# Kernel tuning notes

Measured on AMD Instinct MI355X. Metric: run time of the kernel, lower is better.

## Reference

```python
import jax, jax.numpy as jnp
import numpy as np

EPS = 1e-5  # torch BatchNorm1d default eps


def _bn(x, p):
    # eval-mode batchnorm; p = stacked [gamma, beta, running_mean, running_var], shape [4, C]
    g, b, m, v = p
    return (x - m[:, None]) * jax.lax.rsqrt(v[:, None] + EPS) * g[:, None] + b[:, None]


def _conv(w, x):
    # 1x1 Conv1d == channel matmul: w [O,C], x [B,C,N] -> [B,O,N]
    return jnp.einsum('oc,bcn->bon', w, x)


def _sa(x, qk_w, v_w, v_b, t_w, t_b, bnp):
    # offset self-attention; q_conv.weight is tied to k_conv.weight in the original
    q = jnp.einsum('oc,bcn->bno', qk_w, x)          # [B,N,C/4]
    k = _conv(qk_w, x)                              # [B,C/4,N]
    v = _conv(v_w, x) + v_b[None, :, None]          # [B,C,N]
    attn = jax.nn.softmax(jnp.einsum('bno,bom->bnm', q, k), axis=-1)  # [B,N,N]
    attn = attn / (1e-9 + attn.sum(axis=1, keepdims=True))            # L1 re-norm over dim 1
    x_r = jnp.einsum('bcn,bnm->bcm', v, attn)       # [B,C,N]
    x_r = jax.nn.relu(_bn(_conv(t_w, x - x_r) + t_b[None, :, None], bnp))
    return x + x_r


def setup_inputs():
    key = jax.random.key(0)
    ks = iter(jax.random.split(key, 64))
    def n(shape, s=0.1):
        return jax.random.normal(next(ks), shape, jnp.float32) * s
    def bn_p(c):
        g = jax.random.uniform(next(ks), (c,), jnp.float32, 0.5, 1.5)
        b = n((c,))
        m = n((c,))
        v = jax.random.uniform(next(ks), (c,), jnp.float32, 0.5, 1.5)
        return jnp.stack([g, b, m, v])
    B, C, N = 16, 16, 2048
    return {
        'x': jax.random.normal(next(ks), (B, C, N), jnp.float32),
        'conv1_w': n((128, 16)), 'bn1': bn_p(128),
        'conv2_w': n((16, 128)), 'bn2': bn_p(16),
        'sa_qk_w': n((4, 4, 16)), 'sa_v_w': n((4, 16, 16)), 'sa_v_b': n((4, 16)),
        'sa_trans_w': n((4, 16, 16)), 'sa_trans_b': n((4, 16)),
        'sa_bn': jnp.stack([bn_p(16) for _ in range(4)]),
        'fuse_w': n((128, 64)), 'fuse_bn': bn_p(128),
        'convs1_w': n((512, 264)), 'convs1_b': n((512,)), 'bns1': bn_p(512),
        'convs2_w': n((256, 512)), 'convs2_b': n((256,)), 'bns2': bn_p(256),
        'convs3_w': n((16, 256)), 'convs3_b': n((16,)),
    }


def reference(x, conv1_w, bn1, conv2_w, bn2, sa_qk_w, sa_v_w, sa_v_b,
              sa_trans_w, sa_trans_b, sa_bn, fuse_w, fuse_bn,
              convs1_w, convs1_b, bns1, convs2_w, convs2_b, bns2,
              convs3_w, convs3_b):
    B, _, N = x.shape
    h = jax.nn.relu(_bn(_conv(conv1_w, x), bn1))   # [B,128,N]
    h = jax.nn.relu(_bn(_conv(conv2_w, h), bn2))   # [B,16,N]
    feats = []
    for i in range(4):
        h = _sa(h, sa_qk_w[i], sa_v_w[i], sa_v_b[i], sa_trans_w[i], sa_trans_b[i], sa_bn[i])
        feats.append(h)
    xqq = jnp.concatenate(feats, axis=1)           # [B,64,N]
    xqqw = jax.nn.leaky_relu(_bn(_conv(fuse_w, xqq), fuse_bn), 0.2)  # [B,128,N]
    # faithful to original (including the [1]-indexing quirk):
    x_max = jnp.argmax(xqqw, axis=2)               # [B,128] argmax indices (torch.max(...)[1])
    x_avg = jnp.mean(xqqw, axis=2)[1]              # [128] batch element 1's channel means
    x_max_f = jnp.broadcast_to(x_max.astype(jnp.float32)[:, :, None], (B, 128, N))
    x_avg_f = jnp.broadcast_to(x_avg.reshape(B, -1)[:, :, None], (B, 128 // B, N))
    g = jnp.concatenate([xqqw, x_max_f, x_avg_f], axis=1)  # [B,264,N]
    g = jax.nn.relu(_bn(_conv(convs1_w, g) + convs1_b[None, :, None], bns1))
    # dropout is identity in eval mode
    g = jax.nn.relu(_bn(_conv(convs2_w, g) + convs2_b[None, :, None], bns2))
    return _conv(convs3_w, g) + convs3_b[None, :, None]  # [B,16,N]
```

## Files before the change

kernel.cpp:

```cpp
#include <hip/hip_runtime.h>
#include <stdint.h>

typedef __bf16 bf16_t;
typedef __bf16 bf16x8 __attribute__((ext_vector_type(8)));
typedef __bf16 bf16x4 __attribute__((ext_vector_type(4)));
typedef float f32x4 __attribute__((ext_vector_type(4)));
typedef float f32x2 __attribute__((ext_vector_type(2)));

#define LOG2E 1.4426950408889634f

__device__ __forceinline__ float relu_(float v) { return v > 0.f ? v : 0.f; }

__global__ __launch_bounds__(256) void k_prep(
    const float* __restrict__ convs1_w, const float* __restrict__ convs2_w,
    const float* __restrict__ bn1, const float* __restrict__ bn2,
    const float* __restrict__ sa_bn, const float* __restrict__ sa_trans_b,
    const float* __restrict__ fuse_bn, const float* __restrict__ convs1_b,
    const float* __restrict__ bns1, const float* __restrict__ convs2_b,
    const float* __restrict__ bns2,
    bf16_t* __restrict__ wbuf1, bf16_t* __restrict__ wbuf2, float* __restrict__ params)
{
  int idx = blockIdx.x * 256 + threadIdx.x;
  for (int it = 0; it < 3; ++it) {
    int i = idx + it * 65536;
    if (i < 65536) {
      int o = i >> 7, c = i & 127;
      wbuf1[i] = (bf16_t)convs1_w[o * 264 + c];
    } else if (i < 65536 + 131072) {
      int j = i - 65536;
      wbuf2[j] = (bf16_t)convs2_w[j];
    }
  }
  if (blockIdx.x == 0) {
    for (int t = threadIdx.x; t < 1104; t += 256) {
      float g, be, m, v, extra = 0.f; int so, ho;
      if (t < 128)      { g=bn1[t]; be=bn1[128+t]; m=bn1[256+t]; v=bn1[384+t]; so=t; ho=128+t; }
      else if (t < 144) { int u=t-128; g=bn2[u]; be=bn2[16+u]; m=bn2[32+u]; v=bn2[48+u]; so=256+u; ho=272+u; }
      else if (t < 208) { int u=t-144; int L=u>>4, o=u&15; const float* p=sa_bn+L*64;
                          g=p[o]; be=p[16+o]; m=p[32+o]; v=p[48+o];
                          extra=sa_trans_b[L*16+o]; so=288+u; ho=352+u; }
      else if (t < 336) { int u=t-208; g=fuse_bn[u]; be=fuse_bn[128+u]; m=fuse_bn[256+u]; v=fuse_bn[384+u]; so=416+u; ho=544+u; }
      else if (t < 848) { int u=t-336; g=bns1[u]; be=bns1[512+u]; m=bns1[1024+u]; v=bns1[1536+u]; extra=convs1_b[u]; so=672+u; ho=1184+u; }
      else              { int u=t-848; g=bns2[u]; be=bns2[256+u]; m=bns2[512+u]; v=bns2[768+u]; extra=convs2_b[u]; so=1696+u; ho=1952+u; }
      float sc = g * rsqrtf(v + 1e-5f);
      params[so] = sc;
      params[ho] = (extra - m) * sc + be;
    }
  }
}

__global__ __launch_bounds__(256) void k_convs(const float* __restrict__ x,
    const float* __restrict__ w1, const float* __restrict__ w2,
    const float* __restrict__ params, const float* __restrict__ qk_w,
    const float* __restrict__ v_w, const float* __restrict__ v_b,
    float* __restrict__ h0, float* __restrict__ kbuf, float* __restrict__ vbufT)
{
  __shared__ __align__(16) float xs[16 * 128];
  __shared__ float ws1[128 * 17];
  __shared__ float ws2[16 * 129];
  __shared__ __align__(16) float h1s[128 * 64];
  __shared__ float hcv[128 * 17];
  __shared__ float qk[64], vw[256], vb[16], sc1[128], sh1[128], sc2[16], sh2[16];
  int t = threadIdx.x;
  int bid = blockIdx.x;
  int b = bid >> 4, n0 = (bid & 15) * 128;
  for (int i = t; i < 2048; i += 256) { int c = i >> 7, col = i & 127; xs[c * 128 + col] = x[((size_t)b * 16 + c) * 2048 + n0 + col]; }
  for (int i = t; i < 2048; i += 256) { int o = i >> 4, c = i & 15;  ws1[o * 17 + c]  = w1[i]; }
  for (int i = t; i < 2048; i += 256) { int o = i >> 7, c = i & 127; ws2[o * 129 + c] = w2[i]; }
  if (t < 64) qk[t] = qk_w[t];
  vw[t] = v_w[t];
  if (t < 16) { vb[t] = v_b[t]; sc2[t] = params[256 + t]; sh2[t] = params[272 + t]; }
  if (t < 128) { sc1[t] = params[t]; sh1[t] = params[128 + t]; }
  __syncthreads();
  int colh = t & 63, hi4 = t >> 6;
  int cg = t & 15, og = t >> 4;
  for (int h = 0; h < 2; ++h) {
    int cb = h * 64;
    float xr[16];
#pragma unroll
    for (int c = 0; c < 16; ++c) xr[c] = xs[c * 128 + cb + colh];
#pragma unroll 4
    for (int i = 0; i < 32; ++i) {
      int o = (i << 2) | hi4;
      float s = 0.f;
#pragma unroll
      for (int c = 0; c < 16; ++c) s = fmaf(ws1[o * 17 + c], xr[c], s);
      h1s[o * 64 + colh] = relu_(fmaf(s, sc1[o], sh1[o]));
    }
    __syncthreads();
    float a0 = 0.f, a1 = 0.f, a2 = 0.f, a3 = 0.f;
    for (int c = 0; c < 128; ++c) {
      float4 f = *(const float4*)&h1s[c * 64 + cg * 4];
      float w = ws2[og * 129 + c];
      a0 = fmaf(w, f.x, a0); a1 = fmaf(w, f.y, a1);
      a2 = fmaf(w, f.z, a2); a3 = fmaf(w, f.w, a3);
    }
    float4 v4;
    v4.x = relu_(fmaf(a0, sc2[og], sh2[og]));
    v4.y = relu_(fmaf(a1, sc2[og], sh2[og]));
    v4.z = relu_(fmaf(a2, sc2[og], sh2[og]));
    v4.w = relu_(fmaf(a3, sc2[og], sh2[og]));
    *(float4*)&h0[((size_t)b * 16 + og) * 2048 + n0 + cb + cg * 4] = v4;
    hcv[(cb + cg * 4 + 0) * 17 + og] = v4.x;
    hcv[(cb + cg * 4 + 1) * 17 + og] = v4.y;
    hcv[(cb + cg * 4 + 2) * 17 + og] = v4.z;
    hcv[(cb + cg * 4 + 3) * 17 + og] = v4.w;
    __syncthreads();
  }
  int col = t & 127, ug = t >> 7;
  float hr[16];
#pragma unroll
  for (int c = 0; c < 16; ++c) hr[c] = hcv[col * 17 + c];
#pragma unroll
  for (int i = 0; i < 10; ++i) {
    int u = ug * 10 + i;
    const float* W = (u < 4) ? &qk[u * 16] : &vw[(u - 4) * 16];
    float s = (u < 4) ? 0.f : vb[u - 4];
#pragma unroll
    for (int c = 0; c < 16; ++c) s = fmaf(W[c], hr[c], s);
    if (u < 4) kbuf[((size_t)b * 2048 + n0 + col) * 4 + u] = s;
    else       vbufT[((size_t)b * 2048 + n0 + col) * 16 + (u - 4)] = s;
  }
}

__global__ __launch_bounds__(256) void k_rowstats(const float* __restrict__ kbuf, float* __restrict__ Lpart)
{
  __shared__ float4 kch[256];
  int bid = blockIdx.x;
  int b = bid >> 6, nt = (bid >> 3) & 7, ms = bid & 7;
  int t = threadIdx.x;
  const float4* kb = (const float4*)kbuf + b * 2048;
  kch[t] = kb[ms * 256 + t];
  __syncthreads();
  int n = nt * 256 + t;
  float4 q = kb[n];
  q.x *= LOG2E; q.y *= LOG2E; q.z *= LOG2E; q.w *= LOG2E;
  float L = 0.f;
#pragma unroll 4
  for (int m = 0; m < 256; ++m) {
    float4 k4 = kch[m];
    float s = fmaf(q.x, k4.x, fmaf(q.y, k4.y, fmaf(q.z, k4.z, q.w * k4.w)));
    L += exp2f(s);
  }
  Lpart[((size_t)ms * 16 + b) * 2048 + n] = L;
}

__global__ __launch_bounds__(256) void k_colaccum(const float* __restrict__ kbuf, const float* __restrict__ vbufT,
    const float* __restrict__ Lpart, float* __restrict__ parts)
{
  __shared__ __align__(16) float ku[256 * 8];
  __shared__ __align__(16) float vch[256 * 16];
  int bid = blockIdx.x;
  int b = bid >> 5, mt = (bid >> 3) & 3, ns = bid & 7;
  int t = threadIdx.x;
  {
    int n = ns * 256 + t;
    float4 k4 = ((const float4*)kbuf)[b * 2048 + n];
    float Ls = 0.f;
#pragma unroll
    for (int s = 0; s < 8; ++s) Ls += Lpart[((size_t)s * 16 + b) * 2048 + n];
    *(float4*)&ku[t * 8] = k4;
    ku[t * 8 + 4] = -__log2f(Ls);
    const float4* vp = (const float4*)&vbufT[((size_t)b * 2048 + n) * 16];
    *(float4*)&vch[t * 16 + 0]  = vp[0];
    *(float4*)&vch[t * 16 + 4]  = vp[1];
    *(float4*)&vch[t * 16 + 8]  = vp[2];
    *(float4*)&vch[t * 16 + 12] = vp[3];
  }
  __syncthreads();
  int m0 = mt * 512 + t;
  float4 qa = ((const float4*)kbuf)[b * 2048 + m0];
  float4 qb = ((const float4*)kbuf)[b * 2048 + m0 + 256];
  qa.x *= LOG2E; qa.y *= LOG2E; qa.z *= LOG2E; qa.w *= LOG2E;
  qb.x *= LOG2E; qb.y *= LOG2E; qb.z *= LOG2E; qb.w *= LOG2E;
  f32x2 acc0[8], acc1[8];
#pragma unroll
  for (int j = 0; j < 8; ++j) { acc0[j] = (f32x2){0.f, 0.f}; acc1[j] = (f32x2){0.f, 0.f}; }
  float den0 = 0.f, den1 = 0.f;
#pragma unroll 2
  for (int nn = 0; nn < 256; ++nn) {
    f32x4 k4 = *(const f32x4*)&ku[nn * 8];
    float lg = ku[nn * 8 + 4];
    float s0 = fmaf(qa.x, k4[0], fmaf(qa.y, k4[1], fmaf(qa.z, k4[2], fmaf(qa.w, k4[3], lg))));
    float s1 = fmaf(qb.x, k4[0], fmaf(qb.y, k4[1], fmaf(qb.z, k4[2], fmaf(qb.w, k4[3], lg))));
    float e0 = exp2f(s0), e1 = exp2f(s1);
    den0 += e0; den1 += e1;
    f32x2 ev0 = {e0, e0}, ev1 = {e1, e1};
    const f32x2* vp = (const f32x2*)&vch[nn * 16];
#pragma unroll
    for (int j = 0; j < 8; ++j) { f32x2 v2 = vp[j]; acc0[j] += ev0 * v2; acc1[j] += ev1 * v2; }
  }
  float* p = parts + ((size_t)(ns * 16 + b) * 17) * 2048 + m0;
#pragma unroll
  for (int c = 0; c < 16; ++c) p[(size_t)c * 2048] = acc0[c >> 1][c & 1];
  p[(size_t)16 * 2048] = den0;
  p += 256;
#pragma unroll
  for (int c = 0; c < 16; ++c) p[(size_t)c * 2048] = acc1[c >> 1][c & 1];
  p[(size_t)16 * 2048] = den1;
}

__global__ __launch_bounds__(256) void k_epilogue(const float* __restrict__ parts,
    const float* __restrict__ hin, int hbs, const float* __restrict__ t_w,
    const float* __restrict__ params, int layer, float* __restrict__ hout,
    const float* __restrict__ qk_w, const float* __restrict__ v_w, const float* __restrict__ v_b,
    float* __restrict__ kbuf, float* __restrict__ vbufT)
{
  __shared__ float pd[17 * 64];
  __shared__ float hs[16 * 64];
  __shared__ float dl[16 * 64];
  __shared__ float hv[64 * 17];
  __shared__ float tw[256], qk[64], vw[256], vb[16], sc[16], sh[16];
  int t = threadIdx.x;
  int bid = blockIdx.x;
  int b = bid >> 5, n0 = (bid & 31) * 64;
  tw[t] = t_w[t];
  if (qk_w) { if (t < 64) qk[t] = qk_w[t]; vw[t] = v_w[t]; if (t < 16) vb[t] = v_b[t]; }
  if (t < 16) { sc[t] = params[288 + layer * 16 + t]; sh[t] = params[352 + layer * 16 + t]; }
  for (int i = t; i < 1088; i += 256) {
    int r = i >> 6, c = i & 63;
    float s = 0.f;
#pragma unroll
    for (int sp = 0; sp < 8; ++sp)
      s += parts[((size_t)(sp * 16 + b) * 17 + r) * 2048 + n0 + c];
    pd[i] = s;
  }
  for (int i = t; i < 1024; i += 256) {
    int c = i >> 6, col = i & 63;
    hs[i] = hin[(size_t)b * hbs + (size_t)c * 2048 + n0 + col];
  }
  __syncthreads();
  int col = t & 63, g4 = t >> 6;
  float inv = 1.f / (1e-9f + pd[16 * 64 + col]);
#pragma unroll
  for (int j = 0; j < 4; ++j) {
    int c = g4 * 4 + j;
    dl[c * 64 + col] = hs[c * 64 + col] - pd[c * 64 + col] * inv;
  }
  __syncthreads();
#pragma unroll
  for (int j = 0; j < 4; ++j) {
    int o = g4 * 4 + j;
    float y = 0.f;
#pragma unroll
    for (int c = 0; c < 16; ++c) y = fmaf(tw[o * 16 + c], dl[c * 64 + col], y);
    y = relu_(fmaf(y, sc[o], sh[o]));
    float hh = hs[o * 64 + col] + y;
    hout[(size_t)b * 64 * 2048 + (size_t)o * 2048 + n0 + col] = hh;
    hv[col * 17 + o] = hh;
  }
  if (qk_w) {
    __syncthreads();
    float hr[16];
#pragma unroll
    for (int c = 0; c < 16; ++c) hr[c] = hv[col * 17 + c];
#pragma unroll
    for (int i = 0; i < 5; ++i) {
      int u = g4 * 5 + i;
      const float* W = (u < 4) ? &qk[u * 16] : &vw[(u - 4) * 16];
      float s = (u < 4) ? 0.f : vb[u - 4];
#pragma unroll
      for (int c = 0; c < 16; ++c) s = fmaf(W[c], hr[c], s);
      if (u < 4) kbuf[((size_t)b * 2048 + n0 + col) * 4 + u] = s;
      else       vbufT[((size_t)b * 2048 + n0 + col) * 16 + (u - 4)] = s;
    }
  }
}

__global__ __launch_bounds__(256) void k_fuse(const float* __restrict__ feats, const float* __restrict__ fw,
    const float* __restrict__ params, float* __restrict__ xqqw, bf16_t* __restrict__ gbuf)
{
  __shared__ float ws[128 * 65];
  __shared__ __align__(16) float fst[64 * 64];
  __shared__ float sc[128], sh[128];
  int t = threadIdx.x, bid = blockIdx.x;
  int b = bid >> 5, n0 = (bid & 31) * 64;
  for (int i = t; i < 8192; i += 256) { int o = i >> 6, c = i & 63; ws[o * 65 + c] = fw[i]; }
  for (int i = t; i < 4096; i += 256) { int c = i >> 6, col = i & 63; fst[i] = feats[((size_t)b * 64 + c) * 2048 + n0 + col]; }
  if (t < 128) { sc[t] = params[416 + t]; sh[t] = params[544 + t]; }
  __syncthreads();
  int cg = t & 7, og = t >> 3;
  f32x2 acc[4][4];
#pragma unroll
  for (int oo = 0; oo < 4; ++oo)
#pragma unroll
    for (int j = 0; j < 4; ++j) acc[oo][j] = (f32x2){0.f, 0.f};
  for (int c = 0; c < 64; ++c) {
    const f32x2* fp = (const f32x2*)&fst[c * 64 + cg * 8];
    f32x2 f0 = fp[0], f1 = fp[1], f2v = fp[2], f3 = fp[3];
#pragma unroll
    for (int oo = 0; oo < 4; ++oo) {
      float w = ws[(og * 4 + oo) * 65 + c];
      f32x2 wv = {w, w};
      acc[oo][0] += wv * f0; acc[oo][1] += wv * f1;
      acc[oo][2] += wv * f2v; acc[oo][3] += wv * f3;
    }
  }
  float y[4][8];
#pragma unroll
  for (int oo = 0; oo < 4; ++oo) {
    int o = og * 4 + oo;
    float s0 = sc[o], s1 = sh[o];
#pragma unroll
    for (int j = 0; j < 8; ++j) {
      float v = fmaf(acc[oo][j >> 1][j & 1], s0, s1);
      y[oo][j] = v > 0.f ? v : 0.2f * v;
    }
    float4 v0 = {y[oo][0], y[oo][1], y[oo][2], y[oo][3]};
    float4 v1 = {y[oo][4], y[oo][5], y[oo][6], y[oo][7]};
    *(float4*)&xqqw[((size_t)b * 128 + o) * 2048 + n0 + cg * 8] = v0;
    *(float4*)&xqqw[((size_t)b * 128 + o) * 2048 + n0 + cg * 8 + 4] = v1;
  }
#pragma unroll
  for (int j = 0; j < 8; ++j) {
    int col = n0 + cg * 8 + j;
    bf16x4 pk;
    pk[0] = (bf16_t)y[0][j]; pk[1] = (bf16_t)y[1][j];
    pk[2] = (bf16_t)y[2][j]; pk[3] = (bf16_t)y[3][j];
    *(bf16x4*)&gbuf[((size_t)b * 2048 + col) * 128 + og * 4] = pk;
  }
}

__global__ __launch_bounds__(256) void k_argmax(const float* __restrict__ xqqw,
    float* __restrict__ xmaxf, float* __restrict__ xavg)
{
  __shared__ float sv[256]; __shared__ int si[256]; __shared__ float ss[256];
  int bo = blockIdx.x;
  int b = bo >> 7, o = bo & 127;
  const float* row = xqqw + (size_t)bo * 2048;
  int tid = threadIdx.x;
  float best = -3.4e38f; int bi = 0; float sum = 0.f;
#pragma unroll
  for (int j = 0; j < 8; ++j) {
    int n = j * 256 + tid;
    float v = row[n];
    sum += v;
    if (v > best) { best = v; bi = n; }
  }
  sv[tid] = best; si[tid] = bi; ss[tid] = sum;
  __syncthreads();
  for (int s = 128; s > 0; s >>= 1) {
    if (tid < s) {
      float v2 = sv[tid + s]; int i2 = si[tid + s];
      if (v2 > sv[tid] || (v2 == sv[tid] && i2 < si[tid])) { sv[tid] = v2; si[tid] = i2; }
      ss[tid] += ss[tid + s];
    }
    __syncthreads();
  }
  if (tid == 0) {
    xmaxf[bo] = (float)si[0];
    if (b == 1) xavg[o] = ss[0] * (1.0f / 2048.0f);
  }
}

__global__ __launch_bounds__(256) void k_bias2(const float* __restrict__ w1,
    const float* __restrict__ xmaxf, const float* __restrict__ xavg,
    const float* __restrict__ params, float* __restrict__ bias2)
{
  int id = blockIdx.x * 256 + threadIdx.x;
  int o = id >> 4, b = id & 15;
  const float* wr = w1 + (size_t)o * 264;
  float s = 0.f;
  for (int u = 0; u < 128; ++u) s = fmaf(wr[128 + u], xmaxf[b * 128 + u], s);
#pragma unroll
  for (int u = 0; u < 8; ++u)  s = fmaf(wr[256 + u], xavg[b * 8 + u], s);
  bias2[b * 512 + o] = s * params[672 + o];
}

__global__ __launch_bounds__(256) void k_gemm(const bf16_t* __restrict__ A, const bf16_t* __restrict__ Bm,
    const float* __restrict__ scp, const float* __restrict__ shp, const float* __restrict__ bias2,
    bf16_t* __restrict__ Cout, int M, int K, int mtiles)
{
  __shared__ bf16_t At[128 * 32];
  __shared__ bf16_t Bt[128 * 32];
  int tid = threadIdx.x;
  int mt = blockIdx.x % mtiles, ct = blockIdx.x / mtiles;
  int srow = tid >> 2, scol = (tid & 3) << 3;
  const bf16_t* ga = A  + (size_t)(mt * 128 + srow) * K + scol;
  const bf16_t* gb = Bm + (size_t)(ct * 128 + srow) * K + scol;
  int lane = tid & 63, wave = tid >> 6;
  int wr = (wave >> 1) * 64, wc = (wave & 1) * 64;
  int frow = lane & 15, fk = (lane >> 4) * 8;
  const f32x4 z4 = {0.f, 0.f, 0.f, 0.f};
  f32x4 acc[4][4];
#pragma unroll
  for (int i = 0; i < 4; ++i)
#pragma unroll
    for (int j = 0; j < 4; ++j) acc[i][j] = z4;
  uint4 ra0 = *(const uint4*)ga, ra1 = *(const uint4*)(ga + (size_t)64 * K);
  uint4 rb0 = *(const uint4*)gb, rb1 = *(const uint4*)(gb + (size_t)64 * K);
  int ksteps = K >> 5;
  for (int ks = 0; ks < ksteps; ++ks) {
    __syncthreads();
    *(uint4*)&At[tid * 8] = ra0;  *(uint4*)&At[2048 + tid * 8] = ra1;
    *(uint4*)&Bt[tid * 8] = rb0;  *(uint4*)&Bt[2048 + tid * 8] = rb1;
    __syncthreads();
    if (ks + 1 < ksteps) {
      ra0 = *(const uint4*)(ga + (ks + 1) * 32);
      ra1 = *(const uint4*)(ga + (size_t)64 * K + (ks + 1) * 32);
      rb0 = *(const uint4*)(gb + (ks + 1) * 32);
      rb1 = *(const uint4*)(gb + (size_t)64 * K + (ks + 1) * 32);
    }
    bf16x8 af[4], bfr[4];
#pragma unroll
    for (int i = 0; i < 4; ++i) af[i]  = *(const bf16x8*)&At[(wr + i * 16 + frow) * 32 + fk];
#pragma unroll
    for (int j = 0; j < 4; ++j) bfr[j] = *(const bf16x8*)&Bt[(wc + j * 16 + frow) * 32 + fk];
#pragma unroll
    for (int i = 0; i < 4; ++i)
#pragma unroll
      for (int j = 0; j < 4; ++j)
        acc[i][j] = __builtin_amdgcn_mfma_f32_16x16x32_bf16(af[i], bfr[j], acc[i][j], 0, 0, 0);
  }
  int crow = (lane >> 4) * 4, ccol = lane & 15;
#pragma unroll
  for (int i = 0; i < 4; ++i) {
    int o0 = mt * 128 + wr + i * 16 + crow;
    float s0 = scp[o0], s1 = scp[o0+1], s2 = scp[o0+2], s3 = scp[o0+3];
    float t0 = shp[o0], t1 = shp[o0+1], t2 = shp[o0+2], t3 = shp[o0+3];
#pragma unroll
    for (int j = 0; j < 4; ++j) {
      int bn = ct * 128 + wc + j * 16 + ccol;
      float b0 = 0.f, b1 = 0.f, b2 = 0.f, b3 = 0.f;
      if (bias2) {
        const float* bp = bias2 + (size_t)(bn >> 11) * M + o0;
        b0 = bp[0]; b1 = bp[1]; b2 = bp[2]; b3 = bp[3];
      }
      bf16x4 pk;
      pk[0] = (bf16_t)relu_(fmaf(acc[i][j][0], s0, t0 + b0));
      pk[1] = (bf16_t)relu_(fmaf(acc[i][j][1], s1, t1 + b1));
      pk[2] = (bf16_t)relu_(fmaf(acc[i][j][2], s2, t2 + b2));
      pk[3] = (bf16_t)relu_(fmaf(acc[i][j][3], s3, t3 + b3));
      *(bf16x4*)(Cout + (size_t)bn * M + o0) = pk;
    }
  }
}

__global__ __launch_bounds__(128) void k_gemm3(const bf16_t* __restrict__ g2, const float* __restrict__ w3,
    const float* __restrict__ b3, float* __restrict__ out)
{
  __shared__ float wsT[4096];
  __shared__ float bb[16];
  int tid = threadIdx.x;
  for (int i = tid; i < 4096; i += 128) { int o = i >> 8, k = i & 255; wsT[k * 16 + o] = w3[i]; }
  if (tid < 16) bb[tid] = b3[tid];
  __syncthreads();
  int col = blockIdx.x * 128 + tid;
  int b = col >> 11, n = col & 2047;
  const bf16_t* g = g2 + (size_t)col * 256;
  float acc[16];
#pragma unroll
  for (int o = 0; o < 16; ++o) acc[o] = 0.f;
  for (int k0 = 0; k0 < 256; k0 += 8) {
    bf16x8 gv8 = *(const bf16x8*)(g + k0);
#pragma unroll
    for (int kk = 0; kk < 8; ++kk) {
      float gv = (float)gv8[kk];
      const float* wr = &wsT[(k0 + kk) * 16];
#pragma unroll
      for (int o = 0; o < 16; ++o) acc[o] = fmaf(wr[o], gv, acc[o]);
    }
  }
  float* op = out + (size_t)b * 16 * 2048 + n;
#pragma unroll
  for (int o = 0; o < 16; ++o) op[(size_t)o * 2048] = acc[o] + bb[o];
}

extern "C" void kernel_launch(void* const* d_in, const int* in_sizes, int n_in,
                              void* d_out, int out_size, void* d_ws, size_t ws_size,
                              hipStream_t stream)
{
  const float* x         = (const float*)d_in[0];
  const float* conv1_w   = (const float*)d_in[1];
  const float* bn1       = (const float*)d_in[2];
  const float* conv2_w   = (const float*)d_in[3];
  const float* bn2       = (const float*)d_in[4];
  const float* sa_qk_w   = (const float*)d_in[5];
  const float* sa_v_w    = (const float*)d_in[6];
  const float* sa_v_b    = (const float*)d_in[7];
  const float* sa_trans_w= (const float*)d_in[8];
  const float* sa_trans_b= (const float*)d_in[9];
  const float* sa_bn     = (const float*)d_in[10];
  const float* fuse_w    = (const float*)d_in[11];
  const float* fuse_bn   = (const float*)d_in[12];
  const float* convs1_w  = (const float*)d_in[13];
  const float* convs1_b  = (const float*)d_in[14];
  const float* bns1      = (const float*)d_in[15];
  const float* convs2_w  = (const float*)d_in[16];
  const float* convs2_b  = (const float*)d_in[17];
  const float* bns2      = (const float*)d_in[18];
  const float* convs3_w  = (const float*)d_in[19];
  const float* convs3_b  = (const float*)d_in[20];

  char* ws = (char*)d_ws;
  float*  xqqw  = (float*)(ws + 0);
  float*  feats = (float*)(ws + 16777216);
  float*  h0    = (float*)(ws + 25165824);
  float*  kbuf  = (float*)(ws + 27262976);
  float*  vbufT = (float*)(ws + 27787264);
  float*  Lpart = (float*)(ws + 29884416);
  float*  parts = (float*)(ws + 30932992);
  bf16_t* gbuf  = (bf16_t*)(ws + 48758784);
  bf16_t* g2    = (bf16_t*)(ws + 57147392);
  bf16_t* g1    = (bf16_t*)(ws + 0);
  bf16_t* wbuf1 = (bf16_t*)(ws + 73924608);
  bf16_t* wbuf2 = (bf16_t*)(ws + 74055680);
  float*  params= (float*)(ws + 74317824);
  float*  xmaxf = (float*)(ws + 74334208);
  float*  xavg  = (float*)(ws + 74342400);
  float*  bias2 = (float*)(ws + 74346496);

  k_prep<<<256, 256, 0, stream>>>(convs1_w, convs2_w, bn1, bn2, sa_bn, sa_trans_b, fuse_bn,
                                  convs1_b, bns1, convs2_b, bns2, wbuf1, wbuf2, params);
  k_convs<<<256, 256, 0, stream>>>(x, conv1_w, conv2_w, params, sa_qk_w, sa_v_w, sa_v_b,
                                   h0, kbuf, vbufT);
  for (int i = 0; i < 4; ++i) {
    k_rowstats<<<1024, 256, 0, stream>>>(kbuf, Lpart);
    k_colaccum<<<512, 256, 0, stream>>>(kbuf, vbufT, Lpart, parts);
    const float* hin = (i == 0) ? h0 : (feats + (size_t)(i - 1) * 16 * 2048);
    int hbs = (i == 0) ? 16 * 2048 : 64 * 2048;
    bool last = (i == 3);
    k_epilogue<<<512, 256, 0, stream>>>(parts, hin, hbs, sa_trans_w + i * 256, params, i,
        feats + (size_t)i * 16 * 2048,
        last ? nullptr : sa_qk_w + (i + 1) * 64,
        last ? nullptr : sa_v_w + (i + 1) * 256,
        last ? nullptr : sa_v_b + (i + 1) * 16,
        kbuf, vbufT);
  }
  k_fuse<<<512, 256, 0, stream>>>(feats, fuse_w, params, xqqw, gbuf);
  k_argmax<<<2048, 256, 0, stream>>>(xqqw, xmaxf, xavg);
  k_bias2<<<32, 256, 0, stream>>>(convs1_w, xmaxf, xavg, params, bias2);
  k_gemm<<<1024, 256, 0, stream>>>(wbuf1, gbuf, params + 672, params + 1184, bias2, g1, 512, 128, 4);
  k_gemm<<<512, 256, 0, stream>>>(wbuf2, g1, params + 1696, params + 1952, nullptr, g2, 256, 512, 2);
  k_gemm3<<<256, 128, 0, stream>>>(g2, convs3_w, convs3_b, (float*)d_out);
}
```

Measured before the change: 551.9 us.

## Double grid sizes across conv, attention and final GEMM kernels for more parallelism

Halves the per-block work tile in k_convs, k_rowstats, k_colaccum and k_gemm3 and doubles their grid sizes, splitting the attention key dimension into 16 partial slices instead of 8. The epilogue sums 16 partials using vectorized float4 loads, k_colaccum spreads its shared-memory staging across both thread halves, and its V loads become explicit float4 reads. The workspace layout is rearranged to hold the larger partials buffer. The goal is to fill more compute units and raise occupancy, at the cost of more partial-sum traffic and reduction work.

After: 518.3 us. -6.1%, faster.

```diff
diff --git a/kernel.cpp b/kernel.cpp
--- a/kernel.cpp
+++ b/kernel.cpp
@@ -55,16 +55,16 @@
     const float* __restrict__ v_w, const float* __restrict__ v_b,
     float* __restrict__ h0, float* __restrict__ kbuf, float* __restrict__ vbufT)
 {
-  __shared__ __align__(16) float xs[16 * 128];
+  __shared__ float xs[16 * 64];
   __shared__ float ws1[128 * 17];
   __shared__ float ws2[16 * 129];
   __shared__ __align__(16) float h1s[128 * 64];
-  __shared__ float hcv[128 * 17];
+  __shared__ float hcv[64 * 17];
   __shared__ float qk[64], vw[256], vb[16], sc1[128], sh1[128], sc2[16], sh2[16];
   int t = threadIdx.x;
   int bid = blockIdx.x;
-  int b = bid >> 4, n0 = (bid & 15) * 128;
-  for (int i = t; i < 2048; i += 256) { int c = i >> 7, col = i & 127; xs[c * 128 + col] = x[((size_t)b * 16 + c) * 2048 + n0 + col]; }
+  int b = bid >> 5, n0 = (bid & 31) * 64;
+  for (int i = t; i < 1024; i += 256) { int c = i >> 6, col = i & 63; xs[i] = x[((size_t)b * 16 + c) * 2048 + n0 + col]; }
   for (int i = t; i < 2048; i += 256) { int o = i >> 4, c = i & 15;  ws1[o * 17 + c]  = w1[i]; }
   for (int i = t; i < 2048; i += 256) { int o = i >> 7, c = i & 127; ws2[o * 129 + c] = w2[i]; }
   if (t < 64) qk[t] = qk_w[t];
@@ -72,48 +72,39 @@
   if (t < 16) { vb[t] = v_b[t]; sc2[t] = params[256 + t]; sh2[t] = params[272 + t]; }
   if (t < 128) { sc1[t] = params[t]; sh1[t] = params[128 + t]; }
   __syncthreads();
-  int colh = t & 63, hi4 = t >> 6;
-  int cg = t & 15, og = t >> 4;
-  for (int h = 0; h < 2; ++h) {
-    int cb = h * 64;
-    float xr[16];
-#pragma unroll
-    for (int c = 0; c < 16; ++c) xr[c] = xs[c * 128 + cb + colh];
+  int col = t & 63, og = t >> 6;
+  float xr[16];
+#pragma unroll
+  for (int c = 0; c < 16; ++c) xr[c] = xs[c * 64 + col];
 #pragma unroll 4
-    for (int i = 0; i < 32; ++i) {
-      int o = (i << 2) | hi4;
-      float s = 0.f;
-#pragma unroll
-      for (int c = 0; c < 16; ++c) s = fmaf(ws1[o * 17 + c], xr[c], s);
-      h1s[o * 64 + colh] = relu_(fmaf(s, sc1[o], sh1[o]));
-    }
-    __syncthreads();
-    float a0 = 0.f, a1 = 0.f, a2 = 0.f, a3 = 0.f;
-    for (int c = 0; c < 128; ++c) {
-      float4 f = *(const float4*)&h1s[c * 64 + cg * 4];
-      float w = ws2[og * 129 + c];
-      a0 = fmaf(w, f.x, a0); a1 = fmaf(w, f.y, a1);
-      a2 = fmaf(w, f.z, a2); a3 = fmaf(w, f.w, a3);
-    }
-    float4 v4;
-    v4.x = relu_(fmaf(a0, sc2[og], sh2[og]));
-    v4.y = relu_(fmaf(a1, sc2[og], sh2[og]));
-    v4.z = relu_(fmaf(a2, sc2[og], sh2[og]));
-    v4.w = relu_(fmaf(a3, sc2[og], sh2[og]));
-    *(float4*)&h0[((size_t)b * 16 + og) * 2048 + n0 + cb + cg * 4] = v4;
-    hcv[(cb + cg * 4 + 0) * 17 + og] = v4.x;
-    hcv[(cb + cg * 4 + 1) * 17 + og] = v4.y;
-    hcv[(cb + cg * 4 + 2) * 17 + og] = v4.z;
-    hcv[(cb + cg * 4 + 3) * 17 + og] = v4.w;
-    __syncthreads();
-  }
-  int col = t & 127, ug = t >> 7;
+  for (int i = 0; i < 32; ++i) {
+    int o = og * 32 + i;
+    float s = 0.f;
+#pragma unroll
+    for (int c = 0; c < 16; ++c) s = fmaf(ws1[o * 17 + c], xr[c], s);
+    h1s[o * 64 + col] = relu_(fmaf(s, sc1[o], sh1[o]));
+  }
+  __syncthreads();
+  float a[4] = {0.f, 0.f, 0.f, 0.f};
+  for (int c = 0; c < 128; ++c) {
+    float hv = h1s[c * 64 + col];
+#pragma unroll
+    for (int oo = 0; oo < 4; ++oo) a[oo] = fmaf(ws2[(og * 4 + oo) * 129 + c], hv, a[oo]);
+  }
+#pragma unroll
+  for (int oo = 0; oo < 4; ++oo) {
+    int o = og * 4 + oo;
+    float v = relu_(fmaf(a[oo], sc2[o], sh2[o]));
+    h0[((size_t)b * 16 + o) * 2048 + n0 + col] = v;
+    hcv[col * 17 + o] = v;
+  }
+  __syncthreads();
   float hr[16];
 #pragma unroll
   for (int c = 0; c < 16; ++c) hr[c] = hcv[col * 17 + c];
 #pragma unroll
-  for (int i = 0; i < 10; ++i) {
-    int u = ug * 10 + i;
+  for (int i = 0; i < 5; ++i) {
+    int u = og * 5 + i;
     const float* W = (u < 4) ? &qk[u * 16] : &vw[(u - 4) * 16];
     float s = (u < 4) ? 0.f : vb[u - 4];
 #pragma unroll
@@ -125,19 +116,19 @@
 
 __global__ __launch_bounds__(256) void k_rowstats(const float* __restrict__ kbuf, float* __restrict__ Lpart)
 {
-  __shared__ float4 kch[256];
+  __shared__ float4 kch[128];
   int bid = blockIdx.x;
-  int b = bid >> 6, nt = (bid >> 3) & 7, ms = bid & 7;
+  int b = bid >> 7, nt = (bid >> 4) & 7, ms = bid & 15;
   int t = threadIdx.x;
   const float4* kb = (const float4*)kbuf + b * 2048;
-  kch[t] = kb[ms * 256 + t];
+  if (t < 128) kch[t] = kb[ms * 128 + t];
   __syncthreads();
   int n = nt * 256 + t;
   float4 q = kb[n];
   q.x *= LOG2E; q.y *= LOG2E; q.z *= LOG2E; q.w *= LOG2E;
   float L = 0.f;
 #pragma unroll 4
-  for (int m = 0; m < 256; ++m) {
+  for (int m = 0; m < 128; ++m) {
     float4 k4 = kch[m];
     float s = fmaf(q.x, k4.x, fmaf(q.y, k4.y, fmaf(q.z, k4.z, q.w * k4.w)));
     L += exp2f(s);
@@ -148,24 +139,27 @@
 __global__ __launch_bounds__(256) void k_colaccum(const float* __restrict__ kbuf, const float* __restrict__ vbufT,
     const float* __restrict__ Lpart, float* __restrict__ parts)
 {
-  __shared__ __align__(16) float ku[256 * 8];
-  __shared__ __align__(16) float vch[256 * 16];
+  __shared__ __align__(16) float ku[128 * 8];
+  __shared__ __align__(16) float vch[128 * 16];
   int bid = blockIdx.x;
-  int b = bid >> 5, mt = (bid >> 3) & 3, ns = bid & 7;
+  int b = bid >> 6, mt = (bid >> 4) & 3, ns = bid & 15;
   int t = threadIdx.x;
-  {
-    int n = ns * 256 + t;
+  if (t < 128) {
+    int n = ns * 128 + t;
     float4 k4 = ((const float4*)kbuf)[b * 2048 + n];
     float Ls = 0.f;
 #pragma unroll
-    for (int s = 0; s < 8; ++s) Ls += Lpart[((size_t)s * 16 + b) * 2048 + n];
+    for (int s = 0; s < 16; ++s) Ls += Lpart[((size_t)s * 16 + b) * 2048 + n];
     *(float4*)&ku[t * 8] = k4;
     ku[t * 8 + 4] = -__log2f(Ls);
+  } else {
+    int s = t - 128;
+    int n = ns * 128 + s;
     const float4* vp = (const float4*)&vbufT[((size_t)b * 2048 + n) * 16];
-    *(float4*)&vch[t * 16 + 0]  = vp[0];
-    *(float4*)&vch[t * 16 + 4]  = vp[1];
-    *(float4*)&vch[t * 16 + 8]  = vp[2];
-    *(float4*)&vch[t * 16 + 12] = vp[3];
+    *(float4*)&vch[s * 16 + 0]  = vp[0];
+    *(float4*)&vch[s * 16 + 4]  = vp[1];
+    *(float4*)&vch[s * 16 + 8]  = vp[2];
+    *(float4*)&vch[s * 16 + 12] = vp[3];
   }
   __syncthreads();
   int m0 = mt * 512 + t;
@@ -178,17 +172,26 @@
   for (int j = 0; j < 8; ++j) { acc0[j] = (f32x2){0.f, 0.f}; acc1[j] = (f32x2){0.f, 0.f}; }
   float den0 = 0.f, den1 = 0.f;
 #pragma unroll 2
-  for (int nn = 0; nn < 256; ++nn) {
+  for (int nn = 0; nn < 128; ++nn) {
     f32x4 k4 = *(const f32x4*)&ku[nn * 8];
     float lg = ku[nn * 8 + 4];
     float s0 = fmaf(qa.x, k4[0], fmaf(qa.y, k4[1], fmaf(qa.z, k4[2], fmaf(qa.w, k4[3], lg))));
     float s1 = fmaf(qb.x, k4[0], fmaf(qb.y, k4[1], fmaf(qb.z, k4[2], fmaf(qb.w, k4[3], lg))));
     float e0 = exp2f(s0), e1 = exp2f(s1);
     den0 += e0; den1 += e1;
+    f32x4 va = *(const f32x4*)&vch[nn * 16 + 0];
+    f32x4 vbb = *(const f32x4*)&vch[nn * 16 + 4];
+    f32x4 vc = *(const f32x4*)&vch[nn * 16 + 8];
+    f32x4 vd = *(const f32x4*)&vch[nn * 16 + 12];
     f32x2 ev0 = {e0, e0}, ev1 = {e1, e1};
-    const f32x2* vp = (const f32x2*)&vch[nn * 16];
-#pragma unroll
-    for (int j = 0; j < 8; ++j) { f32x2 v2 = vp[j]; acc0[j] += ev0 * v2; acc1[j] += ev1 * v2; }
+    f32x2 p0 = {va[0], va[1]},  p1 = {va[2], va[3]};
+    f32x2 p2 = {vbb[0], vbb[1]}, p3 = {vbb[2], vbb[3]};
+    f32x2 p4 = {vc[0], vc[1]},  p5 = {vc[2], vc[3]};
+    f32x2 p6 = {vd[0], vd[1]},  p7 = {vd[2], vd[3]};
+    acc0[0] += ev0 * p0; acc0[1] += ev0 * p1; acc0[2] += ev0 * p2; acc0[3] += ev0 * p3;
+    acc0[4] += ev0 * p4; acc0[5] += ev0 * p5; acc0[6] += ev0 * p6; acc0[7] += ev0 * p7;
+    acc1[0] += ev1 * p0; acc1[1] += ev1 * p1; acc1[2] += ev1 * p2; acc1[3] += ev1 * p3;
+    acc1[4] += ev1 * p4; acc1[5] += ev1 * p5; acc1[6] += ev1 * p6; acc1[7] += ev1 * p7;
   }
   float* p = parts + ((size_t)(ns * 16 + b) * 17) * 2048 + m0;
 #pragma unroll
@@ -206,7 +209,7 @@
     const float* __restrict__ qk_w, const float* __restrict__ v_w, const float* __restrict__ v_b,
     float* __restrict__ kbuf, float* __restrict__ vbufT)
 {
-  __shared__ float pd[17 * 64];
+  __shared__ __align__(16) float pd[17 * 64];
   __shared__ float hs[16 * 64];
   __shared__ float dl[16 * 64];
   __shared__ float hv[64 * 17];
@@ -217,13 +220,13 @@
   tw[t] = t_w[t];
   if (qk_w) { if (t < 64) qk[t] = qk_w[t]; vw[t] = v_w[t]; if (t < 16) vb[t] = v_b[t]; }
   if (t < 16) { sc[t] = params[288 + layer * 16 + t]; sh[t] = params[352 + layer * 16 + t]; }
-  for (int i = t; i < 1088; i += 256) {
-    int r = i >> 6, c = i & 63;
-    float s = 0.f;
-#pragma unroll
-    for (int sp = 0; sp < 8; ++sp)
-      s += parts[((size_t)(sp * 16 + b) * 17 + r) * 2048 + n0 + c];
-    pd[i] = s;
+  for (int i = t; i < 272; i += 256) {
+    int r = i >> 4, c4 = (i & 15) << 2;
+    f32x4 s = {0.f, 0.f, 0.f, 0.f};
+#pragma unroll
+    for (int sp = 0; sp < 16; ++sp)
+      s += *(const f32x4*)&parts[((size_t)(sp * 16 + b) * 17 + r) * 2048 + n0 + c4];
+    *(f32x4*)&pd[r * 64 + c4] = s;
   }
   for (int i = t; i < 1024; i += 256) {
     int c = i >> 6, col = i & 63;
@@ -436,34 +439,36 @@
   }
 }
 
-__global__ __launch_bounds__(128) void k_gemm3(const bf16_t* __restrict__ g2, const float* __restrict__ w3,
+__global__ __launch_bounds__(256) void k_gemm3(const bf16_t* __restrict__ g2, const float* __restrict__ w3,
     const float* __restrict__ b3, float* __restrict__ out)
 {
   __shared__ float wsT[4096];
   __shared__ float bb[16];
-  int tid = threadIdx.x;
-  for (int i = tid; i < 4096; i += 128) { int o = i >> 8, k = i & 255; wsT[k * 16 + o] = w3[i]; }
-  if (tid < 16) bb[tid] = b3[tid];
-  __syncthreads();
-  int col = blockIdx.x * 128 + tid;
+  int t = threadIdx.x;
+  for (int i = t; i < 4096; i += 256) { int o = i >> 8, k = i & 255; wsT[k * 16 + o] = w3[i]; }
+  if (t < 16) bb[t] = b3[t];
+  __syncthreads();
+  int col = blockIdx.x * 64 + (t & 63);
+  int og = t >> 6;
   int b = col >> 11, n = col & 2047;
   const bf16_t* g = g2 + (size_t)col * 256;
-  float acc[16];
-#pragma unroll
-  for (int o = 0; o < 16; ++o) acc[o] = 0.f;
+  float acc[4] = {0.f, 0.f, 0.f, 0.f};
   for (int k0 = 0; k0 < 256; k0 += 8) {
     bf16x8 gv8 = *(const bf16x8*)(g + k0);
 #pragma unroll
     for (int kk = 0; kk < 8; ++kk) {
       float gv = (float)gv8[kk];
-      const float* wr = &wsT[(k0 + kk) * 16];
-#pragma unroll
-      for (int o = 0; o < 16; ++o) acc[o] = fmaf(wr[o], gv, acc[o]);
+      const float* wr = &wsT[(k0 + kk) * 16 + og * 4];
+#pragma unroll
+      for (int oo = 0; oo < 4; ++oo) acc[oo] = fmaf(wr[oo], gv, acc[oo]);
     }
   }
   float* op = out + (size_t)b * 16 * 2048 + n;
 #pragma unroll
-  for (int o = 0; o < 16; ++o) op[(size_t)o * 2048] = acc[o] + bb[o];
+  for (int oo = 0; oo < 4; ++oo) {
+    int o = og * 4 + oo;
+    op[(size_t)o * 2048] = acc[oo] + bb[o];
+  }
 }
 
 extern "C" void kernel_launch(void* const* d_in, const int* in_sizes, int n_in,
@@ -499,24 +504,24 @@
   float*  kbuf  = (float*)(ws + 27262976);
   float*  vbufT = (float*)(ws + 27787264);
   float*  Lpart = (float*)(ws + 29884416);
-  float*  parts = (float*)(ws + 30932992);
-  bf16_t* gbuf  = (bf16_t*)(ws + 48758784);
-  bf16_t* g2    = (bf16_t*)(ws + 57147392);
+  float*  parts = (float*)(ws + 31981568);
   bf16_t* g1    = (bf16_t*)(ws + 0);
-  bf16_t* wbuf1 = (bf16_t*)(ws + 73924608);
-  bf16_t* wbuf2 = (bf16_t*)(ws + 74055680);
-  float*  params= (float*)(ws + 74317824);
-  float*  xmaxf = (float*)(ws + 74334208);
-  float*  xavg  = (float*)(ws + 74342400);
-  float*  bias2 = (float*)(ws + 74346496);
+  bf16_t* g2    = (bf16_t*)(ws + 33554432);
+  bf16_t* gbuf  = (bf16_t*)(ws + 50331648);
+  bf16_t* wbuf1 = (bf16_t*)(ws + 67633152);
+  bf16_t* wbuf2 = (bf16_t*)(ws + 67764224);
+  float*  params= (float*)(ws + 68026368);
+  float*  xmaxf = (float*)(ws + 68042752);
+  float*  xavg  = (float*)(ws + 68050944);
+  float*  bias2 = (float*)(ws + 68055040);
 
   k_prep<<<256, 256, 0, stream>>>(convs1_w, convs2_w, bn1, bn2, sa_bn, sa_trans_b, fuse_bn,
                                   convs1_b, bns1, convs2_b, bns2, wbuf1, wbuf2, params);
-  k_convs<<<256, 256, 0, stream>>>(x, conv1_w, conv2_w, params, sa_qk_w, sa_v_w, sa_v_b,
+  k_convs<<<512, 256, 0, stream>>>(x, conv1_w, conv2_w, params, sa_qk_w, sa_v_w, sa_v_b,
                                    h0, kbuf, vbufT);
   for (int i = 0; i < 4; ++i) {
-    k_rowstats<<<1024, 256, 0, stream>>>(kbuf, Lpart);
-    k_colaccum<<<512, 256, 0, stream>>>(kbuf, vbufT, Lpart, parts);
+    k_rowstats<<<2048, 256, 0, stream>>>(kbuf, Lpart);
+    k_colaccum<<<1024, 256, 0, stream>>>(kbuf, vbufT, Lpart, parts);
     const float* hin = (i == 0) ? h0 : (feats + (size_t)(i - 1) * 16 * 2048);
     int hbs = (i == 0) ? 16 * 2048 : 64 * 2048;
     bool last = (i == 3);
@@ -532,5 +537,5 @@
   k_bias2<<<32, 256, 0, stream>>>(convs1_w, xmaxf, xavg, params, bias2);
   k_gemm<<<1024, 256, 0, stream>>>(wbuf1, gbuf, params + 672, params + 1184, bias2, g1, 512, 128, 4);
   k_gemm<<<512, 256, 0, stream>>>(wbuf2, g1, params + 1696, params + 1952, nullptr, g2, 256, 512, 2);
-  k_gemm3<<<256, 128, 0, stream>>>(g2, convs3_w, convs3_b, (float*)d_out);
-}
+  k_gemm3<<<512, 256, 0, stream>>>(g2, convs3_w, convs3_b, (float*)d_out);
+}
```
